# Optimization experiments

Hardware: AMD Instinct MI355X
Metric: run time of the kernel (lower is better)

## Reference

```python
import jax, jax.numpy as jnp
import numpy as np

N = 10000   # nodes
E = 320000  # edges
D = 3000    # input genes
H1, H2 = 1024, 128
F1, F2, F3, F4 = 256, 512, 1024, 2048
BN_EPS = 1e-5

def setup_inputs() -> dict:
    key = jax.random.key(0)
    ks = jax.random.split(key, 30)
    rn = lambda k, s, sc=0.05: jax.random.normal(k, s, dtype=jnp.float32) * sc
    inp = {}
    inp["x"] = jax.random.normal(ks[0], (N, D), dtype=jnp.float32)
    inp["edge_w"] = jax.random.uniform(ks[1], (E,), dtype=jnp.float32)
    inp["W1"] = rn(ks[2], (D, H1))
    inp["W2"] = rn(ks[3], (H1, H2))
    inp["W3"] = rn(ks[4], (H1, H2))
    dims = [(H2, F1), (F1, F2), (F2, F3), (F3, F4), (F4, D)]
    for i, (di, do) in enumerate(dims, start=1):
        inp[f"fc{i}_w"] = rn(ks[4 + i], (di, do))
        inp[f"fc{i}_b"] = jnp.zeros((do,), jnp.float32)
        if i <= 4:
            inp[f"bn{i}_g"] = jnp.ones((do,), jnp.float32)
            inp[f"bn{i}_b"] = jnp.zeros((do,), jnp.float32)
    inp["edge_src"] = jax.random.randint(ks[20], (E,), 0, N)
    inp["edge_dst"] = jax.random.randint(ks[21], (E,), 0, N)
    return inp

def reference(x, edge_w, W1, W2, W3,
              fc1_w, fc1_b, bn1_g, bn1_b,
              fc2_w, fc2_b, bn2_g, bn2_b,
              fc3_w, fc3_b, bn3_g, bn3_b,
              fc4_w, fc4_b, bn4_g, bn4_b,
              fc5_w, fc5_b, edge_src, edge_dst):
    # sparse adjacency matmul: out[dst] += w * h[src]
    def spmm(h):
        return jax.ops.segment_sum(h[edge_src] * edge_w[:, None], edge_dst, num_segments=N)
    # GCN encoder: GraphConvolution = act(adj @ (x @ W)) (dropout inactive in eval)
    h1 = jax.nn.relu(spmm(x @ W1))
    mu = spmm(h1 @ W2)
    logvar = spmm(h1 @ W3)
    z = mu  # eval-mode reparameterize returns mu
    # inner-product adjacency decoder (act = identity)
    adj_rec = z @ z.T
    # FC stack: Linear -> BatchNorm(eval, running mean=0, var=1) -> ReLU
    inv = 1.0 / jnp.sqrt(jnp.float32(1.0 + BN_EPS))
    def fc(h, w, b, g, be):
        return jax.nn.relu((h @ w + b) * inv * g + be)
    o = fc(z, fc1_w, fc1_b, bn1_g, bn1_b)
    o = fc(o, fc2_w, fc2_b, bn2_g, bn2_b)
    o = fc(o, fc3_w, fc3_b, bn3_g, bn3_b)
    o = fc(o, fc4_w, fc4_b, bn4_g, bn4_b)
    x_rec = o @ fc5_w + fc5_b  # fc5: no batchnorm, identity act
    return (adj_rec, mu, logvar, z, x_rec)
```

## Files before the change

kernel.cpp:

```cpp
#include <hip/hip_runtime.h>
#include <stdint.h>

typedef unsigned short ushort_t;
typedef __attribute__((ext_vector_type(8))) short short8;
typedef __attribute__((ext_vector_type(4))) float f32x4;

#define N_NODES 10000
#define MP      10240
#define E_EDGES 320000
#define D_IN    3000
#define K1P     3008
#define H1      1024
#define H2      128

static __device__ __forceinline__ float b2f(ushort_t u) {
  union { uint32_t u; float f; } x; x.u = ((uint32_t)u) << 16; return x.f;
}
static __device__ __forceinline__ ushort_t f2b(float f) {
  union { float f; uint32_t u; } x; x.f = f;
  uint32_t r = x.u + 0x7FFF + ((x.u >> 16) & 1);
  return (ushort_t)(r >> 16);
}

static __device__ __forceinline__ void gload16(const void* g, void* l) {
  __builtin_amdgcn_global_load_lds(
      (const __attribute__((address_space(1))) uint32_t*)g,
      (__attribute__((address_space(3))) uint32_t*)l, 16, 0, 0);
}

__global__ void zero_k(int* p, int n) {
  int i = blockIdx.x * 256 + threadIdx.x;
  if (i < n) p[i] = 0;
}
__global__ void count_k(const int* __restrict__ ed, int* __restrict__ cnt) {
  int e = blockIdx.x * 256 + threadIdx.x;
  if (e < E_EDGES) atomicAdd(&cnt[ed[e]], 1);
}
__global__ void scan_k(const int* __restrict__ cnt, int* __restrict__ rs, int* __restrict__ cur) {
  __shared__ int sums[256];
  int t = threadIdx.x;
  const int per = 40;
  int base = t * per;
  int s = 0;
  for (int i = 0; i < per; i++) { int idx = base + i; if (idx < N_NODES) s += cnt[idx]; }
  sums[t] = s;
  __syncthreads();
  if (t == 0) { int run = 0; for (int i = 0; i < 256; i++) { int v = sums[i]; sums[i] = run; run += v; } }
  __syncthreads();
  int run = sums[t];
  for (int i = 0; i < per; i++) {
    int idx = base + i;
    if (idx < N_NODES) { rs[idx] = run; cur[idx] = run; run += cnt[idx]; }
  }
  if (t == 255) rs[N_NODES] = run;
}
__global__ void fill_k(const int* __restrict__ es, const int* __restrict__ ed,
                       const float* __restrict__ ew,
                       int* __restrict__ cur, int* __restrict__ psrc, float* __restrict__ pw) {
  int e = blockIdx.x * 256 + threadIdx.x;
  if (e >= E_EDGES) return;
  int d = ed[e];
  int pos = atomicAdd(&cur[d], 1);
  psrc[pos] = es[e];
  pw[pos] = ew[e];
}

__global__ void conv_x_k(const float* __restrict__ x, ushort_t* __restrict__ xb) {
  int g = blockIdx.x * 256 + threadIdx.x;
  int row = g / 376;
  int c8 = (g % 376) * 8;
  float v[8];
  if (row < N_NODES && c8 < 3000) {
    const float4 f0 = *(const float4*)(x + (size_t)row * 3000 + c8);
    const float4 f1 = *(const float4*)(x + (size_t)row * 3000 + c8 + 4);
    v[0]=f0.x; v[1]=f0.y; v[2]=f0.z; v[3]=f0.w;
    v[4]=f1.x; v[5]=f1.y; v[6]=f1.z; v[7]=f1.w;
  } else {
#pragma unroll
    for (int i = 0; i < 8; i++) v[i] = 0.f;
  }
  uint32_t o0 = (uint32_t)f2b(v[0]) | ((uint32_t)f2b(v[1]) << 16);
  uint32_t o1 = (uint32_t)f2b(v[2]) | ((uint32_t)f2b(v[3]) << 16);
  uint32_t o2 = (uint32_t)f2b(v[4]) | ((uint32_t)f2b(v[5]) << 16);
  uint32_t o3 = (uint32_t)f2b(v[6]) | ((uint32_t)f2b(v[7]) << 16);
  uint4 ov; ov.x=o0; ov.y=o1; ov.z=o2; ov.w=o3;
  *(uint4*)&xb[(size_t)row * K1P + c8] = ov;
}

struct Seg { const float* src; ushort_t* dst; int K, Nn, Kp, Np, tilesN, blk0; };
struct SegPack { Seg s[8]; };
__global__ void conv_w_all_k(SegPack P) {
  __shared__ float tile[32][33];
  int b = blockIdx.x;
  int si = 0;
#pragma unroll
  for (int i = 1; i < 8; ++i) if (b >= P.s[i].blk0) si = i;
  Seg sg = P.s[si];
  int rel = b - sg.blk0;
  int tk = rel / sg.tilesN, tn = rel % sg.tilesN;
  int tx = threadIdx.x & 31, ty0 = threadIdx.x >> 5;
#pragma unroll
  for (int i = 0; i < 4; ++i) {
    int ty = ty0 + i * 8;
    int k = tk * 32 + ty, n = tn * 32 + tx;
    tile[ty][tx] = (k < sg.K && n < sg.Nn) ? sg.src[(size_t)k * sg.Nn + n] : 0.f;
  }
  __syncthreads();
#pragma unroll
  for (int i = 0; i < 4; ++i) {
    int ty = ty0 + i * 8;
    int n = tn * 32 + ty, k = tk * 32 + tx;
    sg.dst[(size_t)n * sg.Kp + k] = f2b(tile[tx][ty]);
  }
}

template<int EPI>
__global__ __launch_bounds__(256)
void gemm_bt(const ushort_t* __restrict__ A, const ushort_t* __restrict__ BT, int K,
             void* __restrict__ outp, int ldOut, int realM, int realN,
             const float* __restrict__ bias, const float* __restrict__ bng,
             const float* __restrict__ bnb)
{
  __shared__ ushort_t lA[128 * 32];
  __shared__ ushort_t lB[128 * 32];
  const int tid  = threadIdx.x;
  const int row0 = blockIdx.x * 128;
  const int col0 = blockIdx.y * 128;
  const int lane = tid & 63;
  const int wave = tid >> 6;
  const int wr = (wave >> 1) * 64, wc = (wave & 1) * 64;
  const int fr = lane & 15, fq = lane >> 4;

  f32x4 acc[4][4] = {};

  const int rA = tid >> 2;
  const int cA = (tid & 3) * 8;
  const ushort_t* Ab = A  + (size_t)(row0 + rA) * K + cA;
  const ushort_t* Bb = BT + (size_t)(col0 + rA) * K + cA;
  ushort_t* lA0 = &lA[tid * 8];
  ushort_t* lA1 = &lA[2048 + tid * 8];
  ushort_t* lB0 = &lB[tid * 8];
  ushort_t* lB1 = &lB[2048 + tid * 8];
  const size_t rstep = (size_t)64 * K;

  for (int k0 = 0; k0 < K; k0 += 32) {
    gload16(Ab + k0,         lA0);
    gload16(Ab + rstep + k0, lA1);
    gload16(Bb + k0,         lB0);
    gload16(Bb + rstep + k0, lB1);
    __syncthreads();
    short8 af[4], bv[4];
#pragma unroll
    for (int m = 0; m < 4; m++) af[m] = *(const short8*)&lA[(wr + m * 16 + fr) * 32 + fq * 8];
#pragma unroll
    for (int n = 0; n < 4; n++) bv[n] = *(const short8*)&lB[(wc + n * 16 + fr) * 32 + fq * 8];
#pragma unroll
    for (int m = 0; m < 4; m++)
#pragma unroll
      for (int n = 0; n < 4; n++)
        acc[m][n] = __builtin_amdgcn_mfma_f32_16x16x32_bf16(af[m], bv[n], acc[m][n], 0, 0, 0);
    __syncthreads();
  }

  const float inv = 0.9999950000374997f;
#pragma unroll
  for (int n = 0; n < 4; n++) {
    int col = col0 + wc + n * 16 + fr;
    float s = 0.f, t = 0.f, bb = 0.f;
    if (EPI == 1) { s = inv * bng[col]; t = bias[col] * s + bnb[col]; }
    if (EPI == 2) { bb = (col < realN) ? bias[col] : 0.f; }
#pragma unroll
    for (int m = 0; m < 4; m++) {
      int rowb = row0 + wr + m * 16 + fq * 4;
#pragma unroll
      for (int r = 0; r < 4; r++) {
        int row = rowb + r;
        float v = acc[m][n][r];
        if (EPI == 0) {
          ((ushort_t*)outp)[(size_t)row * ldOut + col] = f2b(v);
        } else if (EPI == 1) {
          v = fmaxf(v * s + t, 0.f);
          ((ushort_t*)outp)[(size_t)row * ldOut + col] = f2b(v);
        } else if (EPI == 2) {
          if (row < realM && col < realN)
            ((float*)outp)[(size_t)row * ldOut + col] = v + bb;
        } else {
          if (row < realM && col < realN)
            ((float*)outp)[(size_t)row * ldOut + col] = v;
        }
      }
    }
  }
}

template<int EPI>
__global__ __launch_bounds__(256, 2)
void gemm3(const ushort_t* __restrict__ A, const ushort_t* __restrict__ BT, int K,
           void* __restrict__ outp, int ldOut, int realM, int realN,
           const float* __restrict__ bias, const float* __restrict__ bng,
           const float* __restrict__ bnb)
{
  __shared__ ushort_t lA[3 * 128 * 32];
  __shared__ ushort_t lB[3 * 256 * 32];
  const int tid = threadIdx.x;
  const int wn  = tid >> 6;
  const int fr  = tid & 15, fq = (tid >> 4) & 3;

  int gx = gridDim.x;
  int nwg = gx * gridDim.y;
  int bid = blockIdx.y * gx + blockIdx.x;
  int q8 = nwg >> 3, r8 = nwg & 7;
  int xcd = bid & 7, j = bid >> 3;
  int swz = (xcd < r8 ? xcd * (q8 + 1) : r8 * (q8 + 1) + (xcd - r8) * q8) + j;
  const int row0 = (swz % gx) * 128;
  const int col0 = (swz / gx) * 256;

  f32x4 acc[8][4] = {};

  auto stA = [&](int p, int kt, int r) {
    int c = r * 256 + tid;
    int row = c >> 2, slot = c & 3;
    int ss = slot ^ ((row >> 1) & 3);
    gload16(A + (size_t)(row0 + row) * K + kt * 32 + ss * 8,
            &lA[p * (128 * 32) + c * 8]);
  };
  auto stB = [&](int p, int kt, int r) {
    int c = r * 256 + tid;
    int row = c >> 2, slot = c & 3;
    int ss = slot ^ ((row >> 1) & 3);
    gload16(BT + (size_t)(col0 + row) * K + kt * 32 + ss * 8,
            &lB[p * (256 * 32) + c * 8]);
  };
  auto stage = [&](int p, int kt) {
    stA(p, kt, 0); stA(p, kt, 1);
    stB(p, kt, 0); stB(p, kt, 1); stB(p, kt, 2); stB(p, kt, 3);
  };

  const int NT = K >> 5;
  stage(0, 0);
  stage(1, 1);

  for (int t = 0; t < NT; ++t) {
    const int p = t % 3;
    const int s = (t + 2) % 3;
    const int ts = (t + 2 < NT) ? t + 2 : NT - 1;
    asm volatile("s_waitcnt vmcnt(6)" ::: "memory");
    __builtin_amdgcn_s_barrier();
    asm volatile("" ::: "memory");
    stage(s, ts);

    short8 bf[4], af[8];
#pragma unroll
    for (int n = 0; n < 4; ++n) {
      int rb = wn * 64 + n * 16 + fr;
      bf[n] = *(const short8*)&lB[p * (256 * 32) + rb * 32 + ((fq ^ ((rb >> 1) & 3)) * 8)];
    }
#pragma unroll
    for (int m = 0; m < 8; ++m) {
      int ra = m * 16 + fr;
      af[m] = *(const short8*)&lA[p * (128 * 32) + ra * 32 + ((fq ^ ((ra >> 1) & 3)) * 8)];
    }
    __builtin_amdgcn_s_setprio(1);
#pragma unroll
    for (int m = 0; m < 8; ++m)
#pragma unroll
      for (int n = 0; n < 4; ++n)
        acc[m][n] = __builtin_amdgcn_mfma_f32_16x16x32_bf16(af[m], bf[n], acc[m][n], 0, 0, 0);
    __builtin_amdgcn_s_setprio(0);
    asm volatile("" ::: "memory");
  }

  const float inv = 0.9999950000374997f;
#pragma unroll
  for (int n = 0; n < 4; ++n) {
    int col = col0 + wn * 64 + n * 16 + fr;
    float sc = 0.f, tc = 0.f, bb = 0.f;
    if (EPI == 1) { sc = inv * bng[col]; tc = bias[col] * sc + bnb[col]; }
    if (EPI == 2) { bb = (col < realN) ? bias[col] : 0.f; }
#pragma unroll
    for (int m = 0; m < 8; ++m) {
      int rowb = row0 + m * 16 + fq * 4;
      if (EPI == 4) {
        if (col < realN && rowb < realM) {
          if (rowb + 4 <= realM) {
            float4 v4; v4.x = acc[m][n][0]; v4.y = acc[m][n][1];
            v4.z = acc[m][n][2]; v4.w = acc[m][n][3];
            *(float4*)((float*)outp + (size_t)col * ldOut + rowb) = v4;
          } else {
            for (int r = 0; r < realM - rowb; ++r)
              ((float*)outp)[(size_t)col * ldOut + rowb + r] = acc[m][n][r];
          }
        }
      } else {
#pragma unroll
        for (int r = 0; r < 4; ++r) {
          int row = rowb + r;
          float v = acc[m][n][r];
          if (EPI == 0) {
            ((ushort_t*)outp)[(size_t)row * ldOut + col] = f2b(v);
          } else if (EPI == 1) {
            v = fmaxf(v * sc + tc, 0.f);
            ((ushort_t*)outp)[(size_t)row * ldOut + col] = f2b(v);
          } else if (EPI == 2) {
            if (row < realM && col < realN)
              ((float*)outp)[(size_t)row * ldOut + col] = v + bb;
          }
        }
      }
    }
  }
}

__global__ void spmm1_k(const ushort_t* __restrict__ h, ushort_t* __restrict__ o,
                        const int* __restrict__ rs, const int* __restrict__ psrc,
                        const float* __restrict__ pw) {
  int dst = blockIdx.x;
  int t = threadIdx.x;
  float a0 = 0.f, a1 = 0.f, a2 = 0.f, a3 = 0.f;
  if (dst < N_NODES) {
    int s0 = rs[dst], e0 = rs[dst + 1];
    for (int i = s0; i < e0; ++i) {
      float wv = pw[i];
      uint2 v = *(const uint2*)&h[(size_t)psrc[i] * H1 + t * 4];
      a0 += wv * b2f((ushort_t)(v.x & 0xffff));
      a1 += wv * b2f((ushort_t)(v.x >> 16));
      a2 += wv * b2f((ushort_t)(v.y & 0xffff));
      a3 += wv * b2f((ushort_t)(v.y >> 16));
    }
  }
  uint2 ov;
  ov.x = (uint32_t)f2b(fmaxf(a0, 0.f)) | ((uint32_t)f2b(fmaxf(a1, 0.f)) << 16);
  ov.y = (uint32_t)f2b(fmaxf(a2, 0.f)) | ((uint32_t)f2b(fmaxf(a3, 0.f)) << 16);
  *(uint2*)&o[(size_t)dst * H1 + t * 4] = ov;
}
__global__ void spmm2_k(const ushort_t* __restrict__ pre, float* __restrict__ mu,
                        float* __restrict__ lv, float* __restrict__ zf,
                        ushort_t* __restrict__ zb,
                        const int* __restrict__ rs, const int* __restrict__ psrc,
                        const float* __restrict__ pw) {
  int dst = blockIdx.x;
  int t = threadIdx.x;
  float acc = 0.f;
  if (dst < N_NODES) {
    int s = rs[dst], e = rs[dst + 1];
    for (int i = s; i < e; i++)
      acc += pw[i] * b2f(pre[(size_t)psrc[i] * 256 + t]);
  }
  if (t < 128) {
    zb[(size_t)dst * 128 + t] = f2b(acc);
    if (dst < N_NODES) {
      mu[(size_t)dst * 128 + t] = acc;
      zf[(size_t)dst * 128 + t] = acc;
    }
  } else if (dst < N_NODES) {
    lv[(size_t)dst * 128 + (t - 128)] = acc;
  }
}

extern "C" void kernel_launch(void* const* d_in, const int* in_sizes, int n_in,
                              void* d_out, int out_size, void* d_ws, size_t ws_size,
                              hipStream_t stream) {
  (void)in_sizes; (void)n_in; (void)out_size; (void)ws_size;
  const float* x  = (const float*)d_in[0];
  const float* ew = (const float*)d_in[1];
  const float* W1 = (const float*)d_in[2];
  const float* W2 = (const float*)d_in[3];
  const float* W3 = (const float*)d_in[4];
  const float* fc_w[5] = {(const float*)d_in[5], (const float*)d_in[9],  (const float*)d_in[13], (const float*)d_in[17], (const float*)d_in[21]};
  const float* fc_b[5] = {(const float*)d_in[6], (const float*)d_in[10], (const float*)d_in[14], (const float*)d_in[18], (const float*)d_in[22]};
  const float* bn_g[4] = {(const float*)d_in[7], (const float*)d_in[11], (const float*)d_in[15], (const float*)d_in[19]};
  const float* bn_b[4] = {(const float*)d_in[8], (const float*)d_in[12], (const float*)d_in[16], (const float*)d_in[20]};
  const int* esrc = (const int*)d_in[23];
  const int* edst = (const int*)d_in[24];
  float* out = (float*)d_out;

  float* out_adj = out;
  float* out_mu  = out + (size_t)100000000;
  float* out_lv  = out + (size_t)101280000;
  float* out_z   = out + (size_t)102560000;
  float* out_xr  = out + (size_t)103840000;

  char* w = (char*)d_ws;
  size_t off = 0;
  auto alloc = [&](size_t bytes) { size_t o = off; off = (off + bytes + 255) & ~(size_t)255; return o; };
  int*      cnt  = (int*)(w + alloc(4 * N_NODES));
  int*      rs   = (int*)(w + alloc(4 * (N_NODES + 1)));
  int*      cur  = (int*)(w + alloc(4 * N_NODES));
  int*      psrc = (int*)(w + alloc(4 * E_EDGES));
  float*    pw   = (float*)(w + alloc(4 * E_EDGES));
  ushort_t* w1T  = (ushort_t*)(w + alloc((size_t)2 * 1024 * K1P));
  ushort_t* w23T = (ushort_t*)(w + alloc((size_t)2 * 256 * 1024));
  ushort_t* f1T  = (ushort_t*)(w + alloc((size_t)2 * 256 * 128));
  ushort_t* f2T  = (ushort_t*)(w + alloc((size_t)2 * 512 * 256));
  ushort_t* f3T  = (ushort_t*)(w + alloc((size_t)2 * 1024 * 512));
  ushort_t* f4T  = (ushort_t*)(w + alloc((size_t)2 * 2048 * 1024));
  ushort_t* f5T  = (ushort_t*)(w + alloc((size_t)2 * 3072 * 2048));
  ushort_t* xb   = (ushort_t*)(w + alloc((size_t)2 * MP * K1P));
  ushort_t* xw1b = (ushort_t*)(w + alloc((size_t)2 * MP * H1));
  ushort_t* h1b  = (ushort_t*)(w + alloc((size_t)2 * MP * H1));
  ushort_t* preb = (ushort_t*)(w + alloc((size_t)2 * MP * 256));
  ushort_t* zb   = (ushort_t*)(w + alloc((size_t)2 * MP * 128));
  ushort_t* act1 = xw1b;
  ushort_t* act2 = xb;
  ushort_t* act3 = h1b;
  ushort_t* act4 = xb;

  zero_k<<<(N_NODES + 255) / 256, 256, 0, stream>>>(cnt, N_NODES);
  count_k<<<(E_EDGES + 255) / 256, 256, 0, stream>>>(edst, cnt);
  scan_k<<<1, 256, 0, stream>>>(cnt, rs, cur);
  fill_k<<<(E_EDGES + 255) / 256, 256, 0, stream>>>(esrc, edst, ew, cur, psrc, pw);

  conv_x_k<<<(MP * 376) / 256, 256, 0, stream>>>(x, xb);
  {
    SegPack P;
    int b0 = 0;
    auto mk = [&](const float* s, ushort_t* d, int K, int Nn, int Kp, int Np) {
      Seg sg; sg.src = s; sg.dst = d; sg.K = K; sg.Nn = Nn; sg.Kp = Kp; sg.Np = Np;
      sg.tilesN = Np / 32; sg.blk0 = b0;
      b0 += (Kp / 32) * (Np / 32);
      return sg;
    };
    P.s[0] = mk(W1,      w1T,                       D_IN, 1024, K1P,  1024);
    P.s[1] = mk(W2,      w23T,                      1024, 128,  1024, 128);
    P.s[2] = mk(W3,      w23T + (size_t)128 * 1024, 1024, 128,  1024, 128);
    P.s[3] = mk(fc_w[0], f1T,                       128,  256,  128,  256);
    P.s[4] = mk(fc_w[1], f2T,                       256,  512,  256,  512);
    P.s[5] = mk(fc_w[2], f3T,                       512,  1024, 512,  1024);
    P.s[6] = mk(fc_w[3], f4T,                       1024, 2048, 1024, 2048);
    P.s[7] = mk(fc_w[4], f5T,                       2048, 3000, 2048, 3072);
    conv_w_all_k<<<b0, 256, 0, stream>>>(P);
  }

  dim3 blk2(256);
  gemm3<0><<<dim3(MP / 128, 1024 / 256), blk2, 0, stream>>>(xb, w1T, K1P, xw1b, 1024, MP, 1024, nullptr, nullptr, nullptr);
  spmm1_k<<<dim3(MP), blk2, 0, stream>>>(xw1b, h1b, rs, psrc, pw);
  gemm_bt<0><<<dim3(MP / 128, 2), blk2, 0, stream>>>(h1b, w23T, 1024, preb, 256, MP, 256, nullptr, nullptr, nullptr);
  spmm2_k<<<dim3(MP), blk2, 0, stream>>>(preb, out_mu, out_lv, out_z, zb, rs, psrc, pw);
  gemm3<4><<<dim3(MP / 128, MP / 256), blk2, 0, stream>>>(zb, zb, 128, out_adj, 10000, N_NODES, N_NODES, nullptr, nullptr, nullptr);
  gemm_bt<1><<<dim3(MP / 128, 2), blk2, 0, stream>>>(zb,   f1T, 128,  act1, 256,  MP, 256,  fc_b[0], bn_g[0], bn_b[0]);
  gemm_bt<1><<<dim3(MP / 128, 4), blk2, 0, stream>>>(act1, f2T, 256,  act2, 512,  MP, 512,  fc_b[1], bn_g[1], bn_b[1]);
  gemm3<1><<<dim3(MP / 128, 1024 / 256), blk2, 0, stream>>>(act2, f3T, 512,  act3, 1024, MP, 1024, fc_b[2], bn_g[2], bn_b[2]);
  gemm3<1><<<dim3(MP / 128, 2048 / 256), blk2, 0, stream>>>(act3, f4T, 1024, act4, 2048, MP, 2048, fc_b[3], bn_g[3], bn_b[3]);
  gemm3<2><<<dim3(MP / 128, 3072 / 256), blk2, 0, stream>>>(act4, f5T, 2048, out_xr, 3000, N_NODES, 3000, fc_b[4], nullptr, nullptr);
}
```

Measured before the change: 851.6 us.

## Co-schedule adjacency decoder tiles inside the FC3-FC5 GEMM launches

Removes the standalone z@z^T launch and spreads its 3200 output tiles across the grids of the FC3, FC4 and FC5 GEMMs. Each mixed launch interleaves FC tiles with adjacency tiles by block index, so the memory-bound adjacency stores overlap with the compute-bound FC tiles. The GEMM body is factored into a shared device function. The tile split and the swizzle are hardcoded for 80 row tiles, and the mixed blocks may have uneven runtimes.

New measurement: 854.5 us. Within noise of the previous version (+0.3%).

```diff
diff --git a/kernel.cpp b/kernel.cpp
--- a/kernel.cpp
+++ b/kernel.cpp
@@ -194,26 +194,16 @@
 }
 
 template<int EPI>
-__global__ __launch_bounds__(256, 2)
-void gemm3(const ushort_t* __restrict__ A, const ushort_t* __restrict__ BT, int K,
-           void* __restrict__ outp, int ldOut, int realM, int realN,
-           const float* __restrict__ bias, const float* __restrict__ bng,
-           const float* __restrict__ bnb)
+static __device__ __forceinline__
+void gemm3_body(const ushort_t* __restrict__ A, const ushort_t* __restrict__ BT, int K,
+                void* __restrict__ outp, int ldOut, int realM, int realN,
+                const float* __restrict__ bias, const float* __restrict__ bng,
+                const float* __restrict__ bnb, int row0, int col0,
+                ushort_t* lA, ushort_t* lB)
 {
-  __shared__ ushort_t lA[3 * 128 * 32];
-  __shared__ ushort_t lB[3 * 256 * 32];
   const int tid = threadIdx.x;
   const int wn  = tid >> 6;
   const int fr  = tid & 15, fq = (tid >> 4) & 3;
-
-  int gx = gridDim.x;
-  int nwg = gx * gridDim.y;
-  int bid = blockIdx.y * gx + blockIdx.x;
-  int q8 = nwg >> 3, r8 = nwg & 7;
-  int xcd = bid & 7, j = bid >> 3;
-  int swz = (xcd < r8 ? xcd * (q8 + 1) : r8 * (q8 + 1) + (xcd - r8) * q8) + j;
-  const int row0 = (swz % gx) * 128;
-  const int col0 = (swz / gx) * 256;
 
   f32x4 acc[8][4] = {};
 
@@ -308,6 +298,56 @@
         }
       }
     }
+  }
+}
+
+template<int EPI>
+__global__ __launch_bounds__(256, 2)
+void gemm3(const ushort_t* __restrict__ A, const ushort_t* __restrict__ BT, int K,
+           void* __restrict__ outp, int ldOut, int realM, int realN,
+           const float* __restrict__ bias, const float* __restrict__ bng,
+           const float* __restrict__ bnb)
+{
+  __shared__ ushort_t lA[3 * 128 * 32];
+  __shared__ ushort_t lB[3 * 256 * 32];
+  int gx = gridDim.x;
+  int nwg = gx * gridDim.y;
+  int bid = blockIdx.y * gx + blockIdx.x;
+  int q8 = nwg >> 3, r8 = nwg & 7;
+  int xcd = bid & 7, j = bid >> 3;
+  int swz = (xcd < r8 ? xcd * (q8 + 1) : r8 * (q8 + 1) + (xcd - r8) * q8) + j;
+  const int row0 = (swz % gx) * 128;
+  const int col0 = (swz / gx) * 256;
+  gemm3_body<EPI>(A, BT, K, outp, ldOut, realM, realN, bias, bng, bnb, row0, col0, lA, lB);
+}
+
+template<int EPIFC>
+__global__ __launch_bounds__(256, 2)
+void gemm3_mix(const ushort_t* __restrict__ A, const ushort_t* __restrict__ BT, int K,
+               void* __restrict__ outp, int ldOut, int realM, int realN,
+               const float* __restrict__ bias, const float* __restrict__ bng,
+               const float* __restrict__ bnb,
+               const ushort_t* __restrict__ zbp, float* __restrict__ out_adj,
+               int nFC, int adjBase)
+{
+  __shared__ ushort_t lA[3 * 128 * 32];
+  __shared__ ushort_t lB[3 * 256 * 32];
+  const int T = gridDim.x * gridDim.y;
+  const int b = blockIdx.y * gridDim.x + blockIdx.x;
+  const int F0 = (b * nFC) / T;
+  const int F1 = ((b + 1) * nFC) / T;
+  if (F1 > F0) {
+    int q8 = nFC >> 3;
+    int swz = (F0 & 7) * q8 + (F0 >> 3);
+    int row0 = (swz % 80) * 128;
+    int col0 = (swz / 80) * 256;
+    gemm3_body<EPIFC>(A, BT, K, outp, ldOut, realM, realN, bias, bng, bnb, row0, col0, lA, lB);
+  } else {
+    int adjid = adjBase + (b - F0);
+    if (adjid >= 3200) return;
+    int rowt = adjid % 80, colt = adjid / 80;
+    gemm3_body<4>(zbp, zbp, 128, out_adj, 10000, 10000, 10000,
+                  nullptr, nullptr, nullptr, rowt * 128, colt * 256, lA, lB);
   }
 }
 
@@ -436,10 +476,13 @@
   spmm1_k<<<dim3(MP), blk2, 0, stream>>>(xw1b, h1b, rs, psrc, pw);
   gemm_bt<0><<<dim3(MP / 128, 2), blk2, 0, stream>>>(h1b, w23T, 1024, preb, 256, MP, 256, nullptr, nullptr, nullptr);
   spmm2_k<<<dim3(MP), blk2, 0, stream>>>(preb, out_mu, out_lv, out_z, zb, rs, psrc, pw);
-  gemm3<4><<<dim3(MP / 128, MP / 256), blk2, 0, stream>>>(zb, zb, 128, out_adj, 10000, N_NODES, N_NODES, nullptr, nullptr, nullptr);
+
   gemm_bt<1><<<dim3(MP / 128, 2), blk2, 0, stream>>>(zb,   f1T, 128,  act1, 256,  MP, 256,  fc_b[0], bn_g[0], bn_b[0]);
   gemm_bt<1><<<dim3(MP / 128, 4), blk2, 0, stream>>>(act1, f2T, 256,  act2, 512,  MP, 512,  fc_b[1], bn_g[1], bn_b[1]);
-  gemm3<1><<<dim3(MP / 128, 1024 / 256), blk2, 0, stream>>>(act2, f3T, 512,  act3, 1024, MP, 1024, fc_b[2], bn_g[2], bn_b[2]);
-  gemm3<1><<<dim3(MP / 128, 2048 / 256), blk2, 0, stream>>>(act3, f4T, 1024, act4, 2048, MP, 2048, fc_b[3], bn_g[3], bn_b[3]);
-  gemm3<2><<<dim3(MP / 128, 3072 / 256), blk2, 0, stream>>>(act4, f5T, 2048, out_xr, 3000, N_NODES, 3000, fc_b[4], nullptr, nullptr);
-}
+  gemm3_mix<1><<<dim3(80, 17), blk2, 0, stream>>>(act2, f3T, 512,  act3, 1024, MP, 1024,
+      fc_b[2], bn_g[2], bn_b[2], zb, out_adj, 320, 0);
+  gemm3_mix<1><<<dim3(80, 21), blk2, 0, stream>>>(act3, f4T, 1024, act4, 2048, MP, 2048,
+      fc_b[3], bn_g[3], bn_b[3], zb, out_adj, 640, 1040);
+  gemm3_mix<2><<<dim3(80, 26), blk2, 0, stream>>>(act4, f5T, 2048, out_xr, 3000, N_NODES, 3000,
+      fc_b[4], nullptr, nullptr, zb, out_adj, 960, 2080);
+}
```
